# Kernel optimization log

Measured on AMD Instinct MI355X. Metric: run time of the kernel, lower is better.

The kernel has to match this reference:

```python
import jax, jax.numpy as jnp
import numpy as np
import math

N_HEAD = 16
N_EMBD = 2048

def setup_inputs() -> dict:
    key = jax.random.key(0)
    k1, k2, k3, k4, k5 = jax.random.split(key, 5)
    B, T, C = 4, 2048, N_EMBD
    x = jax.random.normal(k1, (B, T, C), dtype=jnp.float32)
    # torch Linear stores weight [out,in]; we store [in,out] for x @ W
    s_attn = 1.0 / math.sqrt(C)
    w_attn = jax.random.normal(k2, (C, 3 * C), dtype=jnp.float32) * s_attn
    b_attn = jnp.zeros((3 * C,), dtype=jnp.float32)
    w_proj = jax.random.normal(k3, (C, C), dtype=jnp.float32) * s_attn
    b_proj = jnp.zeros((C,), dtype=jnp.float32)
    return {"x": x, "w_attn": w_attn, "b_attn": b_attn,
            "w_proj": w_proj, "b_proj": b_proj}

def reference(x, w_attn, b_attn, w_proj, b_proj):
    B, T, C = x.shape
    H = N_HEAD
    D = C // H
    qkv = x @ w_attn + b_attn                      # [B,T,3C]
    q, k, v = jnp.split(qkv, 3, axis=2)
    q = q.reshape(B, T, H, D).transpose(0, 2, 1, 3)  # [B,H,T,D]
    k = k.reshape(B, T, H, D).transpose(0, 2, 1, 3)
    v = v.reshape(B, T, H, D).transpose(0, 2, 1, 3)
    scale = 1.0 / math.sqrt(D)
    att = jnp.einsum('bhqd,bhkd->bhqk', q, k) * scale  # [B,H,T,T]
    causal = jnp.tril(jnp.ones((T, T), dtype=bool))    # mask slice bias[:, :, FULL_T-T:FULL_T, :FULL_T] with FULL_T==T
    att = jnp.where(causal[None, None], att, -jnp.inf)
    att = jax.nn.softmax(att.astype(jnp.float32), axis=-1).astype(att.dtype)
    y = jnp.einsum('bhqk,bhkd->bhqd', att, v)          # [B,H,T,D]
    y = y.transpose(0, 2, 1, 3).reshape(B, T, C)
    return y @ w_proj + b_proj
```

## Files before the change

kernel.cpp:

```cpp
#include <hip/hip_runtime.h>
#include <hip/hip_bf16.h>

#define NB 4
#define TT 2048
#define CC 2048
#define HH 16
#define DD 128

typedef short bvec8 __attribute__((ext_vector_type(8)));
typedef float fvec4 __attribute__((ext_vector_type(4)));

__device__ __forceinline__ void gload16(const void* g, void* l) {
  __builtin_amdgcn_global_load_lds(
      (__attribute__((address_space(1))) void*)g,
      (__attribute__((address_space(3))) void*)l, 16, 0, 0);
}

__device__ __forceinline__ unsigned short f2bf(float f) {
  union { float f; unsigned int u; } x; x.f = f;
  unsigned int u = x.u;
  return (unsigned short)((u + 0x7FFFu + ((u >> 16) & 1u)) >> 16);
}

__device__ __forceinline__ fvec4 mfma16(bvec8 a, bvec8 b, fvec4 c) {
  return __builtin_amdgcn_mfma_f32_16x16x32_bf16(a, b, c, 0, 0, 0);
}

#define KSC (0.08838834764831845f * 1.4426950408889634f)

__global__ __launch_bounds__(256) void k_cvt(const float* __restrict__ in,
                                             unsigned short* __restrict__ out, int n4) {
  int i = blockIdx.x * 256 + threadIdx.x;
  if (i >= n4) return;
  float4 v = ((const float4*)in)[i];
  ushort4 o;
  o.x = f2bf(v.x); o.y = f2bf(v.y); o.z = f2bf(v.z); o.w = f2bf(v.w);
  ((ushort4*)out)[i] = o;
}

__global__ __launch_bounds__(256) void k_transpose(const float* __restrict__ in,
                                                   unsigned short* __restrict__ out,
                                                   int R, int Cn) {
  __shared__ unsigned short tile[64][65];
  int tC = blockIdx.x * 64, tR = blockIdx.y * 64;
  int t = threadIdx.x;
  for (int i = 0; i < 16; i++) {
    int idx = t + i * 256; int r = idx >> 6, c = idx & 63;
    tile[r][c] = f2bf(in[(size_t)(tR + r) * Cn + tC + c]);
  }
  __syncthreads();
  for (int i = 0; i < 16; i++) {
    int idx = t + i * 256; int r = idx >> 6, c = idx & 63;
    out[(size_t)(tC + r) * R + tR + c] = tile[c][r];
  }
}

template <int EPI>
__global__ __launch_bounds__(512, 2) void k_gemm8(
    const unsigned short* __restrict__ A,
    const unsigned short* __restrict__ Bt,
    const float* __restrict__ bias,
    unsigned short* __restrict__ qk,
    unsigned short* __restrict__ vt,
    float* __restrict__ out) {
  const int K = CC;
  const int nt = K / 64;
  __shared__ unsigned short sm[2][32768];

  int tid = threadIdx.x;
  int wid = tid >> 6, ln = tid & 63, gl = ln >> 4, lo = ln & 15;
  int wr = wid >> 2, wc = wid & 3;

  unsigned nx = gridDim.x;
  unsigned orig = blockIdx.y * nx + blockIdx.x;
  unsigned cpx = (nx * gridDim.y) >> 3;
  unsigned wg = (orig & 7) * cpx + (orig >> 3);
  int m0 = (int)(wg / nx) * 256, n0 = (int)(wg % nx) * 256;

  auto stageA = [&](int buf, int half, int kt) {
#pragma unroll
    for (int j = 0; j < 2; j++) {
      int c = j * 512 + tid;
      int r = c >> 3;
      int kc = (c & 7) ^ (r & 7);
      gload16(A + (size_t)(m0 + half * 128 + r) * K + kt * 64 + kc * 8,
              &sm[buf][(size_t)(half * 1024 + c) * 8]);
    }
  };
  auto stageB = [&](int buf, int half, int kt) {
#pragma unroll
    for (int j = 0; j < 2; j++) {
      int c = j * 512 + tid;
      int r = c >> 3;
      int kc = (c & 7) ^ (r & 7);
      gload16(Bt + (size_t)(n0 + half * 128 + r) * K + kt * 64 + kc * 8,
              &sm[buf][16384 + (size_t)(half * 1024 + c) * 8]);
    }
  };

#define AFRAG(buf, mi, ks) \
  (*(const bvec8*)&sm[buf][(((wr * 128 + (mi) * 16 + lo) * 8) + ((((ks) * 4 + gl)) ^ (lo & 7))) * 8])
#define BFRAG(buf, nj, ks) \
  (*(const bvec8*)&sm[buf][16384 + (((wc * 64 + (nj) * 16 + lo) * 8) + ((((ks) * 4 + gl)) ^ (lo & 7))) * 8])

  fvec4 acc[8][4];
  fvec4 zero = {0.f, 0.f, 0.f, 0.f};
#pragma unroll
  for (int i = 0; i < 8; i++)
#pragma unroll
    for (int j = 0; j < 4; j++) acc[i][j] = zero;

  stageA(0, 0, 0); stageA(0, 1, 0); stageB(0, 0, 0); stageB(0, 1, 0);
  stageA(1, 0, 1); stageA(1, 1, 1);
  asm volatile("s_waitcnt vmcnt(4)" ::: "memory");
  __builtin_amdgcn_sched_barrier(0);
  __builtin_amdgcn_s_barrier();

  for (int t = 0; t < nt; t++) {
    int cur = t & 1;
    bvec8 a0[4], a1[4], a2[4], a3[4], b0[4], b1[4];

#pragma unroll
    for (int mi = 0; mi < 4; mi++) a0[mi] = AFRAG(cur, mi, 0);
#pragma unroll
    for (int nj = 0; nj < 4; nj++) b0[nj] = BFRAG(cur, nj, 0);
    if (t + 1 < nt) stageB(cur ^ 1, 0, t + 1);
    __builtin_amdgcn_s_barrier();
    asm volatile("s_waitcnt lgkmcnt(0)" ::: "memory");
    __builtin_amdgcn_sched_barrier(0);
    __builtin_amdgcn_s_setprio(1);
#pragma unroll
    for (int mi = 0; mi < 4; mi++)
#pragma unroll
      for (int nj = 0; nj < 4; nj++) acc[mi][nj] = mfma16(a0[mi], b0[nj], acc[mi][nj]);
    __builtin_amdgcn_s_setprio(0);
    __builtin_amdgcn_s_barrier();

#pragma unroll
    for (int mi = 0; mi < 4; mi++) a1[mi] = AFRAG(cur, mi + 4, 0);
#pragma unroll
    for (int nj = 0; nj < 4; nj++) b1[nj] = BFRAG(cur, nj, 1);
    if (t + 1 < nt) stageB(cur ^ 1, 1, t + 1);
    __builtin_amdgcn_s_barrier();
    asm volatile("s_waitcnt lgkmcnt(0)" ::: "memory");
    __builtin_amdgcn_sched_barrier(0);
    __builtin_amdgcn_s_setprio(1);
#pragma unroll
    for (int mi = 0; mi < 4; mi++)
#pragma unroll
      for (int nj = 0; nj < 4; nj++) acc[mi + 4][nj] = mfma16(a1[mi], b0[nj], acc[mi + 4][nj]);
    __builtin_amdgcn_s_setprio(0);
    __builtin_amdgcn_s_barrier();

#pragma unroll
    for (int mi = 0; mi < 4; mi++) a2[mi] = AFRAG(cur, mi, 1);
#pragma unroll
    for (int mi = 0; mi < 4; mi++) a3[mi] = AFRAG(cur, mi + 4, 1);
    __builtin_amdgcn_s_barrier();
    asm volatile("s_waitcnt lgkmcnt(0)" ::: "memory");
    __builtin_amdgcn_sched_barrier(0);
    __builtin_amdgcn_s_setprio(1);
#pragma unroll
    for (int mi = 0; mi < 4; mi++)
#pragma unroll
      for (int nj = 0; nj < 4; nj++) acc[mi][nj] = mfma16(a2[mi], b1[nj], acc[mi][nj]);
    __builtin_amdgcn_s_setprio(0);
    __builtin_amdgcn_s_barrier();

    if (t + 2 < nt) { stageA(cur, 0, t + 2); stageA(cur, 1, t + 2); }
    if (t + 2 < nt) {
      asm volatile("s_waitcnt vmcnt(4)" ::: "memory");
    } else {
      asm volatile("s_waitcnt vmcnt(0)" ::: "memory");
    }
    __builtin_amdgcn_sched_barrier(0);
    __builtin_amdgcn_s_barrier();
    __builtin_amdgcn_s_setprio(1);
#pragma unroll
    for (int mi = 0; mi < 4; mi++)
#pragma unroll
      for (int nj = 0; nj < 4; nj++) acc[mi + 4][nj] = mfma16(a3[mi], b1[nj], acc[mi + 4][nj]);
    __builtin_amdgcn_s_setprio(0);
    __builtin_amdgcn_s_barrier();
  }

  if (EPI == 0) {
#pragma unroll
    for (int nj = 0; nj < 4; nj++) {
      int n = n0 + wc * 64 + nj * 16 + lo;
      float bn = bias[n];
      int s = n >> 11, hh = (n >> 7) & 15, d = n & 127;
      float mulv = (s == 1) ? KSC : 1.0f;
#pragma unroll
      for (int mi = 0; mi < 8; mi++) {
        int mb = m0 + wr * 128 + mi * 16 + gl * 4;
        int b = mb >> 11, t0 = mb & 2047;
        if (s < 2) {
          size_t base = ((((size_t)s * NB + b) * HH + hh) * TT) * DD;
#pragma unroll
          for (int r = 0; r < 4; r++)
            qk[base + (size_t)(t0 + r) * DD + d] = f2bf((acc[mi][nj][r] + bn) * mulv);
        } else {
          size_t base = ((((size_t)b * HH + hh) * (TT / 8) + (t0 >> 3)) * DD + d) * 8 + (t0 & 7);
          ushort4 o;
          o.x = f2bf(acc[mi][nj][0] + bn);
          o.y = f2bf(acc[mi][nj][1] + bn);
          o.z = f2bf(acc[mi][nj][2] + bn);
          o.w = f2bf(acc[mi][nj][3] + bn);
          *(ushort4*)&vt[base] = o;
        }
      }
    }
  } else {
#pragma unroll
    for (int nj = 0; nj < 4; nj++) {
      int n = n0 + wc * 64 + nj * 16 + lo;
      float bn = bias[n];
#pragma unroll
      for (int mi = 0; mi < 8; mi++) {
        int m = m0 + wr * 128 + mi * 16 + gl * 4;
#pragma unroll
        for (int r = 0; r < 4; r++) out[(size_t)(m + r) * CC + n] = acc[mi][nj][r] + bn;
      }
    }
  }
#undef AFRAG
#undef BFRAG
}

__global__ __launch_bounds__(256) void k_attn(
    const unsigned short* __restrict__ qk,
    const unsigned short* __restrict__ vt,
    unsigned short* __restrict__ yb) {
  __shared__ unsigned short Ks[2][8192];
  __shared__ unsigned short Vs[2][8192];
  __shared__ unsigned short Ps[4][1024];
  int tid = threadIdx.x, wid = tid >> 6, ln = tid & 63;
  int gl = ln >> 4, lo = ln & 15;
  int qp = blockIdx.x & 15;
  int bh = blockIdx.x >> 4;
  int b = bh >> 4, h = bh & 15;
  const unsigned short* Q  = qk + (((size_t)b * HH + h) * TT) * DD;
  const unsigned short* Kg = qk + ((((size_t)NB + b) * HH + h) * TT) * DD;
  const unsigned short* Vg = vt + (((size_t)b * HH + h) * (TT / 8)) * DD * 8;
  fvec4 zero = {0.f, 0.f, 0.f, 0.f};

  auto stage = [&](int buf, int it) {
    int k0 = it * 64;
#pragma unroll
    for (int j = 0; j < 4; j++) {
      int c = j * 256 + tid;
      int r = c >> 4, cc = c & 15;
      gload16(Kg + (size_t)(k0 + r) * DD + ((cc ^ (r & 7)) * 8), &Ks[buf][(j * 256 + wid * 64) * 8]);
    }
#pragma unroll
    for (int j = 0; j < 4; j++) {
      int c = j * 256 + tid;
      int cc = c >> 7, d = c & 127;
      gload16(Vg + ((size_t)(k0 / 8 + cc) * DD + d) * 8, &Vs[buf][(j * 256 + wid * 64) * 8]);
    }
  };

  for (int pass = 0; pass < 2; pass++) {
    int qt = pass ? (31 - qp) : qp;
    int q0w = qt * 64 + wid * 16;

    bvec8 qf[4];
#pragma unroll
    for (int ks = 0; ks < 4; ks++)
      qf[ks] = *(const bvec8*)(Q + (size_t)(q0w + lo) * DD + ks * 32 + gl * 8);

    fvec4 oacc[8];
#pragma unroll
    for (int i = 0; i < 8; i++) oacc[i] = zero;
    float mrun[4] = {-1e30f, -1e30f, -1e30f, -1e30f};
    float lrun[4] = {0.f, 0.f, 0.f, 0.f};

    int ntiles = qt + 1;
    stage(0, 0);
    asm volatile("s_waitcnt vmcnt(0)" ::: "memory");
    __builtin_amdgcn_sched_barrier(0);
    __builtin_amdgcn_s_barrier();
    __builtin_amdgcn_sched_barrier(0);

    for (int it = 0; it < ntiles; it++) {
      int cur = it & 1;
      int k0 = it * 64;
      if (it + 1 < ntiles) stage(cur ^ 1, it + 1);

      fvec4 sa[4];
#pragma unroll
      for (int fn = 0; fn < 4; fn++) {
        fvec4 s = zero;
#pragma unroll
        for (int ks = 0; ks < 4; ks++) {
          int r = fn * 16 + lo;
          int cd = ks * 4 + gl;
          bvec8 kf = *(const bvec8*)&Ks[cur][(r * 16 + (cd ^ (r & 7))) * 8];
          s = mfma16(qf[ks], kf, s);
        }
        sa[fn] = s;
      }

      float p[4][4], mxl[4];
      bool lastt = (it == qt);
#pragma unroll
      for (int r = 0; r < 4; r++) {
        int qrow = q0w + gl * 4 + r;
        float m = -1e30f;
        if (lastt) {
#pragma unroll
          for (int fn = 0; fn < 4; fn++) {
            int kkg = k0 + fn * 16 + lo;
            float v = (kkg <= qrow) ? sa[fn][r] : -1e30f;
            p[fn][r] = v;
            m = fmaxf(m, v);
          }
        } else {
#pragma unroll
          for (int fn = 0; fn < 4; fn++) {
            float v = sa[fn][r];
            p[fn][r] = v;
            m = fmaxf(m, v);
          }
        }
        mxl[r] = m;
      }
      bool c = (mxl[0] > mrun[0] + 8.f) || (mxl[1] > mrun[1] + 8.f) ||
               (mxl[2] > mrun[2] + 8.f) || (mxl[3] > mrun[3] + 8.f);
      if (__any(c)) {
#pragma unroll
        for (int r = 0; r < 4; r++) {
          float m = mxl[r];
#pragma unroll
          for (int dlt = 1; dlt < 16; dlt <<= 1) m = fmaxf(m, __shfl_xor(m, dlt));
          float mnew = fmaxf(mrun[r], m);
          float corr = exp2f(mrun[r] - mnew);
          mrun[r] = mnew;
          lrun[r] *= corr;
#pragma unroll
          for (int fd = 0; fd < 8; fd++) oacc[fd][r] *= corr;
        }
      }
#pragma unroll
      for (int r = 0; r < 4; r++) {
#pragma unroll
        for (int fn = 0; fn < 4; fn++) {
          float pv = exp2f(p[fn][r] - mrun[r]);
          p[fn][r] = pv;
          lrun[r] += pv;
        }
      }

#pragma unroll
      for (int fn = 0; fn < 4; fn++)
#pragma unroll
        for (int r = 0; r < 4; r++) {
          int qr = gl * 4 + r;
          int kc = fn * 16 + lo;
          Ps[wid][(qr * 8 + (((kc >> 3) ^ (qr & 7)))) * 8 + (kc & 7)] = f2bf(p[fn][r]);
        }

#pragma unroll
      for (int ks2 = 0; ks2 < 2; ks2++) {
        bvec8 pf = *(const bvec8*)&Ps[wid][(lo * 8 + ((ks2 * 4 + gl) ^ (lo & 7))) * 8];
#pragma unroll
        for (int fd = 0; fd < 8; fd++) {
          bvec8 vf = *(const bvec8*)&Vs[cur][((ks2 * 4 + gl) * 128 + fd * 16 + lo) * 8];
          oacc[fd] = mfma16(pf, vf, oacc[fd]);
        }
      }

      asm volatile("s_waitcnt vmcnt(0)" ::: "memory");
      __builtin_amdgcn_sched_barrier(0);
      __builtin_amdgcn_s_barrier();
      __builtin_amdgcn_sched_barrier(0);
    }

#pragma unroll
    for (int r = 0; r < 4; r++) {
      float l = lrun[r];
#pragma unroll
      for (int dlt = 1; dlt < 16; dlt <<= 1) l += __shfl_xor(l, dlt);
      int qrow = q0w + gl * 4 + r;
      float inv = 1.f / l;
#pragma unroll
      for (int fd = 0; fd < 8; fd++) {
        int d = fd * 16 + lo;
        yb[((size_t)b * TT + qrow) * CC + h * DD + d] = f2bf(oacc[fd][r] * inv);
      }
    }
  }
}

extern "C" void kernel_launch(void* const* d_in, const int* in_sizes, int n_in,
                              void* d_out, int out_size, void* d_ws, size_t ws_size,
                              hipStream_t stream) {
  const float* x      = (const float*)d_in[0];
  const float* w_attn = (const float*)d_in[1];
  const float* b_attn = (const float*)d_in[2];
  const float* w_proj = (const float*)d_in[3];
  const float* b_proj = (const float*)d_in[4];
  float* out = (float*)d_out;

  char* ws = (char*)d_ws;
  unsigned short* xb    = (unsigned short*)(ws);
  unsigned short* wab_t = (unsigned short*)(ws + 33554432);
  unsigned short* wpb_t = (unsigned short*)(ws + 58720256);
  unsigned short* qkws  = (unsigned short*)(ws + 67108864);
  unsigned short* vtws  = (unsigned short*)(ws + 134217728);
  unsigned short* ybws  = (unsigned short*)(ws + 167772160);

  hipLaunchKernelGGL(k_cvt, dim3(16384), dim3(256), 0, stream, x, xb, 4194304);
  hipLaunchKernelGGL(k_transpose, dim3(96, 32), dim3(256), 0, stream, w_attn, wab_t, 2048, 6144);
  hipLaunchKernelGGL(k_transpose, dim3(32, 32), dim3(256), 0, stream, w_proj, wpb_t, 2048, 2048);
  hipLaunchKernelGGL((k_gemm8<0>), dim3(24, 32), dim3(512), 0, stream,
                     xb, wab_t, b_attn, qkws, vtws, (float*)nullptr);
  hipLaunchKernelGGL(k_attn, dim3(1024), dim3(256), 0, stream, qkws, vtws, ybws);
  hipLaunchKernelGGL((k_gemm8<1>), dim3(8, 32), dim3(512), 0, stream,
                     ybws, wpb_t, b_proj, (unsigned short*)nullptr, (unsigned short*)nullptr, out);
}
```

Baseline: 480.4 us.

## Double attention query tile per wave and restructure GEMM pipeline barriers

The attention kernel now handles 128-query tiles, with each wave owning two 16-row query fragments. Each K/V fragment loaded from LDS is therefore reused for two MFMA chains, and the grid is halved. The GEMM main loop is reordered to issue all LDS fragment reads up front, prefetch both B halves together, and use fewer barriers per k-step. The aim is less LDS traffic and fewer sync stalls, at the cost of higher register pressure (launch bounds set to 2 blocks), fewer blocks, and the risk of new LDS hazards if the barrier reduction is wrong.

```diff
diff --git a/kernel.cpp b/kernel.cpp
--- a/kernel.cpp
+++ b/kernel.cpp
@@ -112,76 +112,69 @@
 
   stageA(0, 0, 0); stageA(0, 1, 0); stageB(0, 0, 0); stageB(0, 1, 0);
   stageA(1, 0, 1); stageA(1, 1, 1);
-  asm volatile("s_waitcnt vmcnt(4)" ::: "memory");
-  __builtin_amdgcn_sched_barrier(0);
-  __builtin_amdgcn_s_barrier();
 
   for (int t = 0; t < nt; t++) {
     int cur = t & 1;
     bvec8 a0[4], a1[4], a2[4], a3[4], b0[4], b1[4];
 
-#pragma unroll
-    for (int mi = 0; mi < 4; mi++) a0[mi] = AFRAG(cur, mi, 0);
-#pragma unroll
-    for (int nj = 0; nj < 4; nj++) b0[nj] = BFRAG(cur, nj, 0);
-    if (t + 1 < nt) stageB(cur ^ 1, 0, t + 1);
-    __builtin_amdgcn_s_barrier();
-    asm volatile("s_waitcnt lgkmcnt(0)" ::: "memory");
-    __builtin_amdgcn_sched_barrier(0);
-    __builtin_amdgcn_s_setprio(1);
-#pragma unroll
-    for (int mi = 0; mi < 4; mi++)
-#pragma unroll
-      for (int nj = 0; nj < 4; nj++) acc[mi][nj] = mfma16(a0[mi], b0[nj], acc[mi][nj]);
-    __builtin_amdgcn_s_setprio(0);
-    __builtin_amdgcn_s_barrier();
-
-#pragma unroll
-    for (int mi = 0; mi < 4; mi++) a1[mi] = AFRAG(cur, mi + 4, 0);
-#pragma unroll
-    for (int nj = 0; nj < 4; nj++) b1[nj] = BFRAG(cur, nj, 1);
-    if (t + 1 < nt) stageB(cur ^ 1, 1, t + 1);
-    __builtin_amdgcn_s_barrier();
-    asm volatile("s_waitcnt lgkmcnt(0)" ::: "memory");
-    __builtin_amdgcn_sched_barrier(0);
-    __builtin_amdgcn_s_setprio(1);
-#pragma unroll
-    for (int mi = 0; mi < 4; mi++)
-#pragma unroll
-      for (int nj = 0; nj < 4; nj++) acc[mi + 4][nj] = mfma16(a1[mi], b0[nj], acc[mi + 4][nj]);
-    __builtin_amdgcn_s_setprio(0);
-    __builtin_amdgcn_s_barrier();
-
-#pragma unroll
-    for (int mi = 0; mi < 4; mi++) a2[mi] = AFRAG(cur, mi, 1);
-#pragma unroll
-    for (int mi = 0; mi < 4; mi++) a3[mi] = AFRAG(cur, mi + 4, 1);
-    __builtin_amdgcn_s_barrier();
-    asm volatile("s_waitcnt lgkmcnt(0)" ::: "memory");
-    __builtin_amdgcn_sched_barrier(0);
-    __builtin_amdgcn_s_setprio(1);
-#pragma unroll
-    for (int mi = 0; mi < 4; mi++)
-#pragma unroll
-      for (int nj = 0; nj < 4; nj++) acc[mi][nj] = mfma16(a2[mi], b1[nj], acc[mi][nj]);
-    __builtin_amdgcn_s_setprio(0);
-    __builtin_amdgcn_s_barrier();
-
-    if (t + 2 < nt) { stageA(cur, 0, t + 2); stageA(cur, 1, t + 2); }
-    if (t + 2 < nt) {
+    if (t + 1 < nt) {
       asm volatile("s_waitcnt vmcnt(4)" ::: "memory");
     } else {
       asm volatile("s_waitcnt vmcnt(0)" ::: "memory");
     }
     __builtin_amdgcn_sched_barrier(0);
     __builtin_amdgcn_s_barrier();
+    __builtin_amdgcn_sched_barrier(0);
+
+#pragma unroll
+    for (int mi = 0; mi < 4; mi++) a0[mi] = AFRAG(cur, mi, 0);
+#pragma unroll
+    for (int nj = 0; nj < 4; nj++) b0[nj] = BFRAG(cur, nj, 0);
+#pragma unroll
+    for (int mi = 0; mi < 4; mi++) a1[mi] = AFRAG(cur, mi + 4, 0);
+#pragma unroll
+    for (int mi = 0; mi < 4; mi++) a2[mi] = AFRAG(cur, mi, 1);
+#pragma unroll
+    for (int nj = 0; nj < 4; nj++) b1[nj] = BFRAG(cur, nj, 1);
+    if (t + 1 < nt) { stageB(cur ^ 1, 0, t + 1); stageB(cur ^ 1, 1, t + 1); }
+    __builtin_amdgcn_sched_barrier(0);
+
+    __builtin_amdgcn_s_setprio(1);
+#pragma unroll
+    for (int mi = 0; mi < 4; mi++)
+#pragma unroll
+      for (int nj = 0; nj < 4; nj++) acc[mi][nj] = mfma16(a0[mi], b0[nj], acc[mi][nj]);
+    __builtin_amdgcn_s_setprio(0);
+
+#pragma unroll
+    for (int mi = 0; mi < 4; mi++) a3[mi] = AFRAG(cur, mi + 4, 1);
+    __builtin_amdgcn_sched_barrier(0);
+
+    __builtin_amdgcn_s_setprio(1);
+#pragma unroll
+    for (int mi = 0; mi < 4; mi++)
+#pragma unroll
+      for (int nj = 0; nj < 4; nj++) acc[mi + 4][nj] = mfma16(a1[mi], b0[nj], acc[mi + 4][nj]);
+    __builtin_amdgcn_s_setprio(0);
+
+    __builtin_amdgcn_s_setprio(1);
+#pragma unroll
+    for (int mi = 0; mi < 4; mi++)
+#pragma unroll
+      for (int nj = 0; nj < 4; nj++) acc[mi][nj] = mfma16(a2[mi], b1[nj], acc[mi][nj]);
+    __builtin_amdgcn_s_setprio(0);
+
+    asm volatile("s_waitcnt lgkmcnt(0)" ::: "memory");
+    __builtin_amdgcn_sched_barrier(0);
+    __builtin_amdgcn_s_barrier();
+    if (t + 2 < nt) { stageA(cur, 0, t + 2); stageA(cur, 1, t + 2); }
+
     __builtin_amdgcn_s_setprio(1);
 #pragma unroll
     for (int mi = 0; mi < 4; mi++)
 #pragma unroll
       for (int nj = 0; nj < 4; nj++) acc[mi + 4][nj] = mfma16(a3[mi], b1[nj], acc[mi + 4][nj]);
     __builtin_amdgcn_s_setprio(0);
-    __builtin_amdgcn_s_barrier();
   }
 
   if (EPI == 0) {
@@ -228,17 +221,17 @@
 #undef BFRAG
 }
 
-__global__ __launch_bounds__(256) void k_attn(
+__global__ __launch_bounds__(256, 2) void k_attn(
     const unsigned short* __restrict__ qk,
     const unsigned short* __restrict__ vt,
     unsigned short* __restrict__ yb) {
   __shared__ unsigned short Ks[2][8192];
   __shared__ unsigned short Vs[2][8192];
-  __shared__ unsigned short Ps[4][1024];
+  __shared__ unsigned short Ps[4][2048];
   int tid = threadIdx.x, wid = tid >> 6, ln = tid & 63;
   int gl = ln >> 4, lo = ln & 15;
-  int qp = blockIdx.x & 15;
-  int bh = blockIdx.x >> 4;
+  int qp = blockIdx.x & 7;
+  int bh = blockIdx.x >> 3;
   int b = bh >> 4, h = bh & 15;
   const unsigned short* Q  = qk + (((size_t)b * HH + h) * TT) * DD;
   const unsigned short* Kg = qk + ((((size_t)NB + b) * HH + h) * TT) * DD;
@@ -261,22 +254,81 @@
     }
   };
 
+  auto smax = [&](fvec4 (&sa)[4], float (&mr)[4], float (&lr)[4], fvec4 (&oa)[8],
+                  int q0m, int k0, bool domask, int psoff) {
+    float p[4][4], mxl[4];
+#pragma unroll
+    for (int r = 0; r < 4; r++) {
+      int qrow = q0m + gl * 4 + r;
+      float m = -1e30f;
+      if (domask) {
+#pragma unroll
+        for (int fn = 0; fn < 4; fn++) {
+          int kkg = k0 + fn * 16 + lo;
+          float v = (kkg <= qrow) ? sa[fn][r] : -1e30f;
+          p[fn][r] = v; m = fmaxf(m, v);
+        }
+      } else {
+#pragma unroll
+        for (int fn = 0; fn < 4; fn++) {
+          float v = sa[fn][r];
+          p[fn][r] = v; m = fmaxf(m, v);
+        }
+      }
+      mxl[r] = m;
+    }
+    bool c = (mxl[0] > mr[0] + 8.f) || (mxl[1] > mr[1] + 8.f) ||
+             (mxl[2] > mr[2] + 8.f) || (mxl[3] > mr[3] + 8.f);
+    if (__any(c)) {
+#pragma unroll
+      for (int r = 0; r < 4; r++) {
+        float m = mxl[r];
+#pragma unroll
+        for (int dlt = 1; dlt < 16; dlt <<= 1) m = fmaxf(m, __shfl_xor(m, dlt));
+        float mnew = fmaxf(mr[r], m);
+        float corr = exp2f(mr[r] - mnew);
+        mr[r] = mnew; lr[r] *= corr;
+#pragma unroll
+        for (int fd = 0; fd < 8; fd++) oa[fd][r] *= corr;
+      }
+    }
+#pragma unroll
+    for (int r = 0; r < 4; r++)
+#pragma unroll
+      for (int fn = 0; fn < 4; fn++) {
+        float pv = exp2f(p[fn][r] - mr[r]);
+        p[fn][r] = pv; lr[r] += pv;
+      }
+#pragma unroll
+    for (int fn = 0; fn < 4; fn++)
+#pragma unroll
+      for (int r = 0; r < 4; r++) {
+        int qr = gl * 4 + r;
+        int kc = fn * 16 + lo;
+        Ps[wid][psoff + (qr * 8 + ((kc >> 3) ^ (qr & 7))) * 8 + (kc & 7)] = f2bf(p[fn][r]);
+      }
+  };
+
   for (int pass = 0; pass < 2; pass++) {
-    int qt = pass ? (31 - qp) : qp;
-    int q0w = qt * 64 + wid * 16;
-
-    bvec8 qf[4];
-#pragma unroll
-    for (int ks = 0; ks < 4; ks++)
-      qf[ks] = *(const bvec8*)(Q + (size_t)(q0w + lo) * DD + ks * 32 + gl * 8);
-
-    fvec4 oacc[8];
-#pragma unroll
-    for (int i = 0; i < 8; i++) oacc[i] = zero;
-    float mrun[4] = {-1e30f, -1e30f, -1e30f, -1e30f};
-    float lrun[4] = {0.f, 0.f, 0.f, 0.f};
-
-    int ntiles = qt + 1;
+    int qt = pass ? (15 - qp) : qp;
+    int q0w = qt * 128 + wid * 32;
+
+    bvec8 qf0[4], qf1[4];
+#pragma unroll
+    for (int ks = 0; ks < 4; ks++) {
+      qf0[ks] = *(const bvec8*)(Q + (size_t)(q0w + lo) * DD + ks * 32 + gl * 8);
+      qf1[ks] = *(const bvec8*)(Q + (size_t)(q0w + 16 + lo) * DD + ks * 32 + gl * 8);
+    }
+
+    fvec4 oacc0[8], oacc1[8];
+#pragma unroll
+    for (int i = 0; i < 8; i++) { oacc0[i] = zero; oacc1[i] = zero; }
+    float mr0[4] = {-1e30f, -1e30f, -1e30f, -1e30f};
+    float mr1[4] = {-1e30f, -1e30f, -1e30f, -1e30f};
+    float lr0[4] = {0.f, 0.f, 0.f, 0.f};
+    float lr1[4] = {0.f, 0.f, 0.f, 0.f};
+
+    int ntiles = 2 * qt + 2;
     stage(0, 0);
     asm volatile("s_waitcnt vmcnt(0)" ::: "memory");
     __builtin_amdgcn_sched_barrier(0);
@@ -288,86 +340,33 @@
       int k0 = it * 64;
       if (it + 1 < ntiles) stage(cur ^ 1, it + 1);
 
-      fvec4 sa[4];
+      fvec4 sa0[4], sa1[4];
 #pragma unroll
       for (int fn = 0; fn < 4; fn++) {
-        fvec4 s = zero;
+        fvec4 s0 = zero, s1 = zero;
 #pragma unroll
         for (int ks = 0; ks < 4; ks++) {
           int r = fn * 16 + lo;
           int cd = ks * 4 + gl;
           bvec8 kf = *(const bvec8*)&Ks[cur][(r * 16 + (cd ^ (r & 7))) * 8];
-          s = mfma16(qf[ks], kf, s);
+          s0 = mfma16(qf0[ks], kf, s0);
+          s1 = mfma16(qf1[ks], kf, s1);
         }
-        sa[fn] = s;
-      }
-
-      float p[4][4], mxl[4];
-      bool lastt = (it == qt);
-#pragma unroll
-      for (int r = 0; r < 4; r++) {
-        int qrow = q0w + gl * 4 + r;
-        float m = -1e30f;
-        if (lastt) {
-#pragma unroll
-          for (int fn = 0; fn < 4; fn++) {
-            int kkg = k0 + fn * 16 + lo;
-            float v = (kkg <= qrow) ? sa[fn][r] : -1e30f;
-            p[fn][r] = v;
-            m = fmaxf(m, v);
-          }
-        } else {
-#pragma unroll
-          for (int fn = 0; fn < 4; fn++) {
-            float v = sa[fn][r];
-            p[fn][r] = v;
-            m = fmaxf(m, v);
-          }
-        }
-        mxl[r] = m;
-      }
-      bool c = (mxl[0] > mrun[0] + 8.f) || (mxl[1] > mrun[1] + 8.f) ||
-               (mxl[2] > mrun[2] + 8.f) || (mxl[3] > mrun[3] + 8.f);
-      if (__any(c)) {
-#pragma unroll
-        for (int r = 0; r < 4; r++) {
-          float m = mxl[r];
-#pragma unroll
-          for (int dlt = 1; dlt < 16; dlt <<= 1) m = fmaxf(m, __shfl_xor(m, dlt));
-          float mnew = fmaxf(mrun[r], m);
-          float corr = exp2f(mrun[r] - mnew);
-          mrun[r] = mnew;
-          lrun[r] *= corr;
-#pragma unroll
-          for (int fd = 0; fd < 8; fd++) oacc[fd][r] *= corr;
-        }
-      }
-#pragma unroll
-      for (int r = 0; r < 4; r++) {
-#pragma unroll
-        for (int fn = 0; fn < 4; fn++) {
-          float pv = exp2f(p[fn][r] - mrun[r]);
-          p[fn][r] = pv;
-          lrun[r] += pv;
-        }
-      }
-
-#pragma unroll
-      for (int fn = 0; fn < 4; fn++)
-#pragma unroll
-        for (int r = 0; r < 4; r++) {
-          int qr = gl * 4 + r;
-          int kc = fn * 16 + lo;
-          Ps[wid][(qr * 8 + (((kc >> 3) ^ (qr & 7)))) * 8 + (kc & 7)] = f2bf(p[fn][r]);
-        }
+        sa0[fn] = s0; sa1[fn] = s1;
+      }
+
+      smax(sa0, mr0, lr0, oacc0, q0w,      k0, (k0 + 63) > q0w,        0);
+      smax(sa1, mr1, lr1, oacc1, q0w + 16, k0, (k0 + 63) > (q0w + 16), 1024);
 
 #pragma unroll
       for (int ks2 = 0; ks2 < 2; ks2++) {
-        bvec8 pf = *(const bvec8*)&Ps[wid][(lo * 8 + ((ks2 * 4 + gl) ^ (lo & 7))) * 8];
+        bvec8 pf0 = *(const bvec8*)&Ps[wid][(lo * 8 + ((ks2 * 4 + gl) ^ (lo & 7))) * 8];
+        bvec8 pf1 = *(const bvec8*)&Ps[wid][1024 + (lo * 8 + ((ks2 * 4 + gl) ^ (lo & 7))) * 8];
 #pragma unroll
         for (int fd = 0; fd < 8; fd++) {
           bvec8 vf = *(const bvec8*)&Vs[cur][((ks2 * 4 + gl) * 128 + fd * 16 + lo) * 8];
-          oacc[fd] = mfma16(pf, vf, oacc[fd]);
+          oacc0[fd] = mfma16(pf0, vf, oacc0[fd]);
+          oacc1[fd] = mfma16(pf1, vf, oacc1[fd]);
         }
       }
 
@@ -379,15 +378,20 @@
 
 #pragma unroll
     for (int r = 0; r < 4; r++) {
-      float l = lrun[r];
-#pragma unroll
-      for (int dlt = 1; dlt < 16; dlt <<= 1) l += __shfl_xor(l, dlt);
-      int qrow = q0w + gl * 4 + r;
-      float inv = 1.f / l;
+      float l0 = lr0[r], l1 = lr1[r];
+#pragma unroll
+      for (int dlt = 1; dlt < 16; dlt <<= 1) {
+        l0 += __shfl_xor(l0, dlt);
+        l1 += __shfl_xor(l1, dlt);
+      }
+      int qrow0 = q0w + gl * 4 + r;
+      int qrow1 = q0w + 16 + gl * 4 + r;
+      float inv0 = 1.f / l0, inv1 = 1.f / l1;
 #pragma unroll
       for (int fd = 0; fd < 8; fd++) {
         int d = fd * 16 + lo;
-        yb[((size_t)b * TT + qrow) * CC + h * DD + d] = f2bf(oacc[fd][r] * inv);
+        yb[((size_t)b * TT + qrow0) * CC + h * DD + d] = f2bf(oacc0[fd][r] * inv0);
+        yb[((size_t)b * TT + qrow1) * CC + h * DD + d] = f2bf(oacc1[fd][r] * inv1);
       }
     }
   }
@@ -416,7 +420,7 @@
   hipLaunchKernelGGL(k_transpose, dim3(32, 32), dim3(256), 0, stream, w_proj, wpb_t, 2048, 2048);
   hipLaunchKernelGGL((k_gemm8<0>), dim3(24, 32), dim3(512), 0, stream,
                      xb, wab_t, b_attn, qkws, vtws, (float*)nullptr);
-  hipLaunchKernelGGL(k_attn, dim3(1024), dim3(256), 0, stream, qkws, vtws, ybws);
+  hipLaunchKernelGGL(k_attn, dim3(512), dim3(256), 0, stream, qkws, vtws, ybws);
   hipLaunchKernelGGL((k_gemm8<1>), dim3(8, 32), dim3(512), 0, stream,
                      ybws, wpb_t, b_proj, (unsigned short*)nullptr, (unsigned short*)nullptr, out);
 }
```

New measurement: 448.4 us. 1.07x faster.
